# Kernel optimization log

Measured on AMD Instinct MI355X. Metric: run time of the kernel, lower is better.

The kernel has to match this reference:

```python
import jax, jax.numpy as jnp
import numpy as np

P = 16        # patch_size
SP = 8        # shift_pixels = int(patch_size * shift_ratio)
EPS = 1e-5    # torch LayerNorm default eps


def _bilinear_shift(img, sx, sy):
    """Replicates F.grid_sample(bilinear, zeros padding, align_corners=False)
    with a pure translation grid: out[y, x] = img[y + sy, x + sx] (bilinear)."""
    B, C, H, W = img.shape
    ys = jnp.arange(H, dtype=img.dtype) + jnp.asarray(sy, img.dtype)
    xs = jnp.arange(W, dtype=img.dtype) + jnp.asarray(sx, img.dtype)
    y0 = jnp.floor(ys)
    x0 = jnp.floor(xs)
    wy = ys - y0  # [H]
    wx = xs - x0  # [W]

    def gather(iy, ix):
        valid = ((iy >= 0) & (iy < H))[:, None] & ((ix >= 0) & (ix < W))[None, :]
        iyc = jnp.clip(iy, 0, H - 1).astype(jnp.int32)
        ixc = jnp.clip(ix, 0, W - 1).astype(jnp.int32)
        v = img[:, :, iyc][:, :, :, ixc]  # [B, C, H, W]
        return v * valid.astype(img.dtype)

    w00 = (1 - wy)[:, None] * (1 - wx)[None, :]
    w01 = (1 - wy)[:, None] * wx[None, :]
    w10 = wy[:, None] * (1 - wx)[None, :]
    w11 = wy[:, None] * wx[None, :]
    return (w00 * gather(y0, x0) + w01 * gather(y0, x0 + 1)
            + w10 * gather(y0 + 1, x0) + w11 * gather(y0 + 1, x0 + 1))


def reference(x, ln_gamma, ln_beta, w, b):
    B, C, H, W = x.shape
    # Original bug: shift_y = (shift_x * 2 / W) * 2 / H, so the effective
    # vertical pixel shift is ty*H/2 = 2*SP/W (sign of shift_x; dy ignored).
    ty_pix = 2.0 * SP / W
    right_up = _bilinear_shift(x, +SP, +ty_pix)
    left_up = _bilinear_shift(x, -SP, -ty_pix)
    right_down = _bilinear_shift(x, +SP, +ty_pix)
    left_down = _bilinear_shift(x, -SP, -ty_pix)
    xc = jnp.concatenate([x, left_up, right_up, left_down, right_down], axis=1)  # [B, 5C, H, W]
    C5 = xc.shape[1]
    h, ww = H // P, W // P
    # Rearrange 'B C (p1 h) (p2 w) -> B (h w) (C p1 p2)'  (p1/p2 are OUTER factors)
    p = xc.reshape(B, C5, P, h, P, ww)
    p = p.transpose(0, 3, 5, 1, 2, 4).reshape(B, h * ww, C5 * P * P)  # [B, 196, 3840]
    # LayerNorm (biased variance, as in torch)
    mu = p.mean(axis=-1, keepdims=True)
    var = p.var(axis=-1, keepdims=True)
    p = (p - mu) * jax.lax.rsqrt(var + EPS) * ln_gamma + ln_beta
    # Linear
    return p @ w + b  # [B, 196, 768]


def setup_inputs() -> dict:
    key = jax.random.key(0)
    k1, k2 = jax.random.split(key)
    d_in = P * P * 5 * 3  # 3840
    d_model = 768
    return {
        "x": jax.random.normal(k1, (64, 3, 224, 224), dtype=jnp.float32),
        "ln_gamma": jnp.ones((d_in,), dtype=jnp.float32),
        "ln_beta": jnp.zeros((d_in,), dtype=jnp.float32),
        "w": jax.random.normal(k2, (d_in, d_model), dtype=jnp.float32) / np.sqrt(d_in),
        "b": jnp.zeros((d_model,), dtype=jnp.float32),
    }
```

## Files before the change

kernel.cpp:

```cpp
#include <hip/hip_runtime.h>


typedef short bf16x8 __attribute__((ext_vector_type(8)));
typedef unsigned short u16x8 __attribute__((ext_vector_type(8)));
typedef float f32x4 __attribute__((ext_vector_type(4)));

#define GLOBAL_AS __attribute__((address_space(1)))
#define LDS_AS __attribute__((address_space(3)))

__device__ __forceinline__ unsigned short f2bf(float f) {
  union { float f; unsigned int u; } v;
  v.f = f;
  unsigned int u = v.u;
  unsigned int r = (u + 0x7FFFu + ((u >> 16) & 1u)) >> 16;
  return (unsigned short)r;
}

__global__ __launch_bounds__(512) void spt_prep(
    const float* __restrict__ x, const float* __restrict__ gamma,
    const float* __restrict__ beta, const float* __restrict__ w,
    unsigned short* __restrict__ V, float2* __restrict__ stats,
    unsigned short* __restrict__ w2t, float* __restrict__ Gp,
    float* __restrict__ Bp)
{
  __shared__ __align__(16) char smem[79072];
  const int t = threadIdx.x;

  if (blockIdx.x < 896) {
    unsigned short* slab = (unsigned short*)smem;
    float* sred = (float*)(smem + 64736);
    float* qred = sred + 8 * 224;
    const int orig = blockIdx.x;
    const int bi = (orig & 7) * 112 + (orig >> 3);
    const int b = bi / 14, hi = bi % 14;
    const float TW = 16.0f / 224.0f;

    const int q = t % 56;
    const int grp = t / 56;
    const int x4 = q * 4;

    int sloff[4];
    {
      int wi = x4 % 14, p2 = x4 / 14;
      #pragma unroll
      for (int j = 0; j < 4; ++j) {
        sloff[j] = wi * 2312 + p2;
        if (++wi == 14) { wi = 0; ++p2; }
      }
    }

    if (grp < 8) {
      f32x4 sAcc = {0.f, 0.f, 0.f, 0.f}, qAcc = {0.f, 0.f, 0.f, 0.f};
      #pragma unroll
      for (int it = 0; it < 6; ++it) {
        const int cp = grp * 6 + it;
        const int c = cp >> 4, p1 = cp & 15;
        const int y = p1 * 14 + hi;
        const float* row = x + ((size_t)(b * 3 + c)) * 50176 + (size_t)y * 224;
        const f32x4 xv = *(const f32x4*)(row + x4);
        f32x4 ra = {0.f,0.f,0.f,0.f}, rb = {0.f,0.f,0.f,0.f};
        f32x4 la = {0.f,0.f,0.f,0.f}, lb = {0.f,0.f,0.f,0.f};
        if (q < 54) {
          ra = *(const f32x4*)(row + x4 + 8);
          if (y < 223) rb = *(const f32x4*)(row + x4 + 8 + 224);
        }
        if (q >= 2) {
          la = *(const f32x4*)(row + x4 - 8);
          if (y > 0) lb = *(const f32x4*)(row + x4 - 8 - 224);
        }
        const f32x4 rv = (1.0f - TW) * ra + TW * rb;
        const f32x4 lv = (1.0f - TW) * la + TW * lb;
        sAcc += xv + 2.0f * (lv + rv);
        qAcc += xv * xv + 2.0f * (lv * lv + rv * rv);
        const int kb = c * 256 + p1 * 16;
        #pragma unroll
        for (int j = 0; j < 4; ++j) {
          slab[sloff[j] + kb]        = f2bf(xv[j]);
          slab[sloff[j] + kb + 768]  = f2bf(lv[j]);
          slab[sloff[j] + kb + 1536] = f2bf(rv[j]);
        }
      }
      #pragma unroll
      for (int j = 0; j < 4; ++j) {
        sred[grp * 224 + x4 + j] = sAcc[j];
        qred[grp * 224 + x4 + j] = qAcc[j];
      }
    }
    __syncthreads();

    if (t < 224) {
      float ss = 0.f, qq = 0.f;
      #pragma unroll
      for (int g = 0; g < 8; ++g) { ss += sred[g * 224 + t]; qq += qred[g * 224 + t]; }
      sred[t] = ss;
      qred[t] = qq;
    }
    __syncthreads();

    const int tok0 = b * 196 + hi * 14;
    if (t < 14) {
      float S = 0.f, Q = 0.f;
      #pragma unroll
      for (int p = 0; p < 16; ++p) { S += sred[t + 14 * p]; Q += qred[t + 14 * p]; }
      const float mu = S / 3840.f;
      const float var = Q / 3840.f - mu * mu;
      const float r = rsqrtf(var + 1e-5f);
      stats[tok0 + t] = make_float2(r, -mu * r);
    }

    for (int i = t; i < 14 * 288; i += 512) {
      const int wi2 = i / 288, off = i % 288;
      *(u16x8*)&V[(size_t)(tok0 + wi2) * 2304 + off * 8] =
          *(const u16x8*)&slab[wi2 * 2312 + off * 8];
    }
  } else {
    float* tileF = (float*)smem;
    const int bx = blockIdx.x - 896;
    const int fx = bx / 3;
    const int fy = bx % 3;
    const int half = t >> 8;
    const int tt = t & 255;
    const int j = fy * 256 + tt;
    const int f2blk = fx * 32 + half * 16;

    float gacc = 0.f, bacc = 0.f;
    #pragma unroll
    for (int i = 0; i < 16; ++i) {
      const int f2 = f2blk + i;
      const int g = f2 / 768;
      const int rem = f2 % 768;
      float v, bv;
      if (g == 0) {
        const int f = rem;
        const float wv = w[(size_t)f * 768 + j];
        v = gamma[f] * wv;
        bv = beta[f] * wv;
      } else if (g == 1) {
        const int fa = 768 + rem, fb = 2304 + rem;
        const float wa = w[(size_t)fa * 768 + j], wb = w[(size_t)fb * 768 + j];
        v = gamma[fa] * wa + gamma[fb] * wb;
        bv = beta[fa] * wa + beta[fb] * wb;
      } else {
        const int fa = 1536 + rem, fb = 3072 + rem;
        const float wa = w[(size_t)fa * 768 + j], wb = w[(size_t)fb * 768 + j];
        v = gamma[fa] * wa + gamma[fb] * wb;
        bv = beta[fa] * wa + beta[fb] * wb;
      }
      tileF[(half * 16 + i) * 257 + tt] = v;
      gacc += v;
      bacc += bv;
    }
    __syncthreads();
    u16x8 lo, hi;
    #pragma unroll
    for (int i = 0; i < 8; ++i) {
      lo[i] = f2bf(tileF[(half * 16 + i) * 257 + tt]);
      hi[i] = f2bf(tileF[(half * 16 + 8 + i) * 257 + tt]);
    }
    unsigned short* dst = w2t + (size_t)j * 2304 + f2blk;
    *(u16x8*)dst = lo;
    *(u16x8*)(dst + 8) = hi;
    Gp[(fx * 2 + half) * 768 + j] = gacc;
    Bp[(fx * 2 + half) * 768 + j] = bacc;
  }
}

__global__ __launch_bounds__(256) void spt_gb(
    const float* __restrict__ Gp, const float* __restrict__ Bp,
    const float* __restrict__ bvec, float* __restrict__ G, float* __restrict__ Bt)
{
  const int j = blockIdx.x * 256 + threadIdx.x;
  float g = 0.f, bb = 0.f;
  for (int i = 0; i < 144; ++i) {
    g += Gp[i * 768 + j];
    bb += Bp[i * 768 + j];
  }
  G[j] = g;
  Bt[j] = bb + bvec[j];
}

__global__ __launch_bounds__(256, 2) void spt_gemm(
    const unsigned short* __restrict__ V, const unsigned short* __restrict__ w2t,
    const float2* __restrict__ stats, const float* __restrict__ G,
    const float* __restrict__ Bt, float* __restrict__ out)
{
  __shared__ unsigned short Alds[2][224 * 64];
  __shared__ unsigned short Blds[2][96 * 64];

  const int orig = blockIdx.x;
  const int wgid = (orig & 7) * 56 + (orig >> 3);
  const int m0 = (wgid >> 3) * 224;
  const int n0 = (wgid & 7) * 96;
  const int t = threadIdx.x;
  const int w = t >> 6, l = t & 63;
  const int wr = w >> 1;
  const int wn = w & 1;

  f32x4 acc[7][3] = {};

#define STAGE(pb, kt)                                                          \
  {                                                                            \
    const int k0s = (kt) << 6;                                                 \
    _Pragma("unroll") for (int i = 0; i < 7; ++i) {                            \
      const int c = i * 256 + t;                                               \
      const int row = c >> 3;                                                  \
      const int srcel = (((c & 7) ^ (row & 7)) << 3);                          \
      const unsigned short* ga = V + (size_t)(m0 + row) * 2304 + k0s + srcel;  \
      __builtin_amdgcn_global_load_lds((const GLOBAL_AS unsigned int*)ga,      \
          (LDS_AS unsigned int*)&Alds[pb][i * 2048 + w * 512], 16, 0, 0);      \
    }                                                                          \
    _Pragma("unroll") for (int i = 0; i < 3; ++i) {                            \
      const int c = i * 256 + t;                                               \
      const int row = c >> 3;                                                  \
      const int srcel = (((c & 7) ^ (row & 7)) << 3);                          \
      const unsigned short* gb = w2t + (size_t)(n0 + row) * 2304 + k0s + srcel;\
      __builtin_amdgcn_global_load_lds((const GLOBAL_AS unsigned int*)gb,      \
          (LDS_AS unsigned int*)&Blds[pb][i * 2048 + w * 512], 16, 0, 0);      \
    }                                                                          \
  }

#define COMPUTE(pb)                                                            \
  {                                                                            \
    const int lane15 = l & 15;                                                 \
    const int kcol = (l >> 4) << 4;                                            \
    bf16x8 bF[2][3], aF[2][7];                                                 \
    _Pragma("unroll") for (int kk = 0; kk < 2; ++kk) {                         \
      const int kb = kk * 64 + kcol;                                           \
      _Pragma("unroll") for (int n = 0; n < 3; ++n) {                          \
        const int row = wn * 48 + n * 16 + lane15;                             \
        const int phys = row * 128 + (kb ^ ((row & 7) << 4));                  \
        bF[kk][n] = *(const bf16x8*)&Blds[pb][phys >> 1];                      \
      }                                                                        \
      _Pragma("unroll") for (int m = 0; m < 7; ++m) {                          \
        const int row = wr * 112 + m * 16 + lane15;                            \
        const int phys = row * 128 + (kb ^ ((row & 7) << 4));                  \
        aF[kk][m] = *(const bf16x8*)&Alds[pb][phys >> 1];                      \
      }                                                                        \
    }                                                                          \
    __builtin_amdgcn_s_setprio(1);                                             \
    _Pragma("unroll") for (int kk = 0; kk < 2; ++kk)                           \
      _Pragma("unroll") for (int m = 0; m < 7; ++m)                            \
        _Pragma("unroll") for (int n = 0; n < 3; ++n)                          \
          acc[m][n] = __builtin_amdgcn_mfma_f32_16x16x32_bf16(aF[kk][m],       \
                          bF[kk][n], acc[m][n], 0, 0, 0);                      \
    __builtin_amdgcn_s_setprio(0);                                             \
  }

  STAGE(0, 0);
  int pb = 0;
  for (int kt = 0; kt < 35; ++kt) {
    STAGE(pb ^ 1, kt + 1);
    asm volatile("s_waitcnt vmcnt(10)\n\ts_barrier" ::: "memory");
    COMPUTE(pb);
    asm volatile("s_barrier" ::: "memory");
    pb ^= 1;
  }
  asm volatile("s_waitcnt vmcnt(0)\n\ts_barrier" ::: "memory");
  COMPUTE(pb);

  const int lane15 = l & 15;
  const int lg = (l >> 4) * 4;
  #pragma unroll
  for (int m = 0; m < 7; ++m) {
    const int rowb = m0 + wr * 112 + m * 16 + lg;
    float2 st[4];
    #pragma unroll
    for (int r = 0; r < 4; ++r) st[r] = stats[rowb + r];
    #pragma unroll
    for (int n = 0; n < 3; ++n) {
      const int col = n0 + wn * 48 + n * 16 + lane15;
      const float Gc = G[col];
      const float Bc = Bt[col];
      #pragma unroll
      for (int r = 0; r < 4; ++r) {
        out[(size_t)(rowb + r) * 768 + col] = st[r].x * acc[m][n][r] + st[r].y * Gc + Bc;
      }
    }
  }
#undef STAGE
#undef COMPUTE
}

extern "C" void kernel_launch(void* const* d_in, const int* in_sizes, int n_in,
                              void* d_out, int out_size, void* d_ws, size_t ws_size,
                              hipStream_t stream) {
  const float* x     = (const float*)d_in[0];
  const float* gamma = (const float*)d_in[1];
  const float* beta  = (const float*)d_in[2];
  const float* w     = (const float*)d_in[3];
  const float* bvec  = (const float*)d_in[4];
  float* out = (float*)d_out;

  char* ws = (char*)d_ws;
  unsigned short* V   = (unsigned short*)(ws);
  unsigned short* w2t = (unsigned short*)(ws + 57802752);
  float2* stats       = (float2*)(ws + 61341696);
  float* G            = (float*)(ws + 61442048);
  float* Bt           = (float*)(ws + 61445120);
  float* Gp           = (float*)(ws + 61448192);
  float* Bp           = (float*)(ws + 61890560);

  spt_prep<<<1112, 512, 0, stream>>>(x, gamma, beta, w, V, stats, w2t, Gp, Bp);
  spt_gb<<<3, 256, 0, stream>>>(Gp, Bp, bvec, G, Bt);
  spt_gemm<<<448, 256, 0, stream>>>(V, w2t, stats, G, Bt, out);
}
```

Before: 90.26 us.

## Split prep blocks per channel to shrink LDS and raise occupancy

Each prep block now handles one channel of a token row instead of all three. This cuts the LDS slab from about 79KB to 36KB, adds a min-blocks-per-CU launch bound, and triples the number of prep blocks. Per-channel partial sums and sums of squares are written to workspace, and the LayerNorm stats are finished in extra blocks of the small reduction kernel. The goal is more resident waves to hide global-load latency, at the cost of extra partial-stat traffic and narrower, strided V writes.

```diff
diff --git a/kernel.cpp b/kernel.cpp
--- a/kernel.cpp
+++ b/kernel.cpp
@@ -16,23 +16,25 @@
   return (unsigned short)r;
 }
 
-__global__ __launch_bounds__(512) void spt_prep(
+__global__ __launch_bounds__(512, 6) void spt_prep(
     const float* __restrict__ x, const float* __restrict__ gamma,
     const float* __restrict__ beta, const float* __restrict__ w,
-    unsigned short* __restrict__ V, float2* __restrict__ stats,
-    unsigned short* __restrict__ w2t, float* __restrict__ Gp,
-    float* __restrict__ Bp)
+    unsigned short* __restrict__ V, float* __restrict__ Sp,
+    float* __restrict__ Qp, unsigned short* __restrict__ w2t,
+    float* __restrict__ Gp, float* __restrict__ Bp)
 {
-  __shared__ __align__(16) char smem[79072];
+  __shared__ __align__(16) char smem[36064];
   const int t = threadIdx.x;
-
-  if (blockIdx.x < 896) {
+  const int xcd = blockIdx.x & 7;
+  const int local = blockIdx.x >> 3;
+
+  if (local < 336) {
     unsigned short* slab = (unsigned short*)smem;
-    float* sred = (float*)(smem + 64736);
-    float* qred = sred + 8 * 224;
-    const int orig = blockIdx.x;
-    const int bi = (orig & 7) * 112 + (orig >> 3);
-    const int b = bi / 14, hi = bi % 14;
+    float* sred = (float*)(smem + 21728);
+    float* qred = sred + 1792;
+    const int bi = xcd * 336 + local;
+    const int th = bi / 3, c = bi % 3;
+    const int b = th / 14, hi = th % 14;
     const float TW = 16.0f / 224.0f;
 
     const int q = t % 56;
@@ -44,7 +46,7 @@
       int wi = x4 % 14, p2 = x4 / 14;
       #pragma unroll
       for (int j = 0; j < 4; ++j) {
-        sloff[j] = wi * 2312 + p2;
+        sloff[j] = wi * 776 + p2;
         if (++wi == 14) { wi = 0; ++p2; }
       }
     }
@@ -52,9 +54,8 @@
     if (grp < 8) {
       f32x4 sAcc = {0.f, 0.f, 0.f, 0.f}, qAcc = {0.f, 0.f, 0.f, 0.f};
       #pragma unroll
-      for (int it = 0; it < 6; ++it) {
-        const int cp = grp * 6 + it;
-        const int c = cp >> 4, p1 = cp & 15;
+      for (int it = 0; it < 2; ++it) {
+        const int p1 = grp * 2 + it;
         const int y = p1 * 14 + hi;
         const float* row = x + ((size_t)(b * 3 + c)) * 50176 + (size_t)y * 224;
         const f32x4 xv = *(const f32x4*)(row + x4);
@@ -72,12 +73,12 @@
         const f32x4 lv = (1.0f - TW) * la + TW * lb;
         sAcc += xv + 2.0f * (lv + rv);
         qAcc += xv * xv + 2.0f * (lv * lv + rv * rv);
-        const int kb = c * 256 + p1 * 16;
+        const int kb = p1 * 16;
         #pragma unroll
         for (int j = 0; j < 4; ++j) {
           slab[sloff[j] + kb]        = f2bf(xv[j]);
-          slab[sloff[j] + kb + 768]  = f2bf(lv[j]);
-          slab[sloff[j] + kb + 1536] = f2bf(rv[j]);
+          slab[sloff[j] + kb + 256]  = f2bf(lv[j]);
+          slab[sloff[j] + kb + 512]  = f2bf(rv[j]);
         }
       }
       #pragma unroll
@@ -102,22 +103,21 @@
       float S = 0.f, Q = 0.f;
       #pragma unroll
       for (int p = 0; p < 16; ++p) { S += sred[t + 14 * p]; Q += qred[t + 14 * p]; }
-      const float mu = S / 3840.f;
-      const float var = Q / 3840.f - mu * mu;
-      const float r = rsqrtf(var + 1e-5f);
-      stats[tok0 + t] = make_float2(r, -mu * r);
-    }
-
-    for (int i = t; i < 14 * 288; i += 512) {
-      const int wi2 = i / 288, off = i % 288;
-      *(u16x8*)&V[(size_t)(tok0 + wi2) * 2304 + off * 8] =
-          *(const u16x8*)&slab[wi2 * 2312 + off * 8];
+      Sp[c * 12544 + tok0 + t] = S;
+      Qp[c * 12544 + tok0 + t] = Q;
+    }
+
+    for (int i = t; i < 1344; i += 512) {
+      const int wi2 = i / 96, s = i % 96;
+      const int g = s >> 5, i8 = s & 31;
+      *(u16x8*)&V[(size_t)(tok0 + wi2) * 2304 + g * 768 + c * 256 + i8 * 8] =
+          *(const u16x8*)&slab[wi2 * 776 + g * 256 + i8 * 8];
     }
   } else {
     float* tileF = (float*)smem;
-    const int bx = blockIdx.x - 896;
-    const int fx = bx / 3;
-    const int fy = bx % 3;
+    const int fu = xcd * 27 + (local - 336);
+    const int fx = fu / 3;
+    const int fy = fu % 3;
     const int half = t >> 8;
     const int tt = t & 255;
     const int j = fy * 256 + tt;
@@ -167,16 +167,29 @@
 
 __global__ __launch_bounds__(256) void spt_gb(
     const float* __restrict__ Gp, const float* __restrict__ Bp,
-    const float* __restrict__ bvec, float* __restrict__ G, float* __restrict__ Bt)
+    const float* __restrict__ bvec, const float* __restrict__ Sp,
+    const float* __restrict__ Qp, float* __restrict__ G,
+    float* __restrict__ Bt, float2* __restrict__ stats)
 {
-  const int j = blockIdx.x * 256 + threadIdx.x;
-  float g = 0.f, bb = 0.f;
-  for (int i = 0; i < 144; ++i) {
-    g += Gp[i * 768 + j];
-    bb += Bp[i * 768 + j];
-  }
-  G[j] = g;
-  Bt[j] = bb + bvec[j];
+  const int t = threadIdx.x;
+  if (blockIdx.x < 3) {
+    const int j = blockIdx.x * 256 + t;
+    float g = 0.f, bb = 0.f;
+    for (int i = 0; i < 144; ++i) {
+      g += Gp[i * 768 + j];
+      bb += Bp[i * 768 + j];
+    }
+    G[j] = g;
+    Bt[j] = bb + bvec[j];
+  } else {
+    const int tok = (blockIdx.x - 3) * 256 + t;
+    const float S = Sp[tok] + Sp[12544 + tok] + Sp[25088 + tok];
+    const float Q = Qp[tok] + Qp[12544 + tok] + Qp[25088 + tok];
+    const float mu = S / 3840.f;
+    const float var = Q / 3840.f - mu * mu;
+    const float r = rsqrtf(var + 1e-5f);
+    stats[tok] = make_float2(r, -mu * r);
+  }
 }
 
 __global__ __launch_bounds__(256, 2) void spt_gemm(
@@ -299,8 +312,10 @@
   float* Bt           = (float*)(ws + 61445120);
   float* Gp           = (float*)(ws + 61448192);
   float* Bp           = (float*)(ws + 61890560);
-
-  spt_prep<<<1112, 512, 0, stream>>>(x, gamma, beta, w, V, stats, w2t, Gp, Bp);
-  spt_gb<<<3, 256, 0, stream>>>(Gp, Bp, bvec, G, Bt);
+  float* Sp           = (float*)(ws + 62332928);
+  float* Qp           = (float*)(ws + 62483456);
+
+  spt_prep<<<2904, 512, 0, stream>>>(x, gamma, beta, w, V, Sp, Qp, w2t, Gp, Bp);
+  spt_gb<<<52, 256, 0, stream>>>(Gp, Bp, bvec, Sp, Qp, G, Bt, stats);
   spt_gemm<<<448, 256, 0, stream>>>(V, w2t, stats, G, Bt, out);
 }
```

After: 86.08 us (median of 2 runs). 1.05x faster.
